# Optimization experiments

Hardware: AMD Instinct MI355X
Metric: run time of the kernel (lower is better)

Reference implementation:

```python
import jax, jax.numpy as jnp
import numpy as np

EPS = 1e-5


def _gcn_conv(h, W, b, src, dst, norm, N):
    # h: (B, N, F_in) -> linear transform then normalized neighbor aggregation
    h = h @ W                                  # (B, N, H)
    msg = h[:, src, :] * norm[None, :, None]   # gather + edge norm, (B, E, H)
    agg = jax.vmap(lambda m: jax.ops.segment_sum(m, dst, num_segments=N))(msg)
    return agg + b


def _batchnorm(h, gamma, beta):
    # BatchNorm1d over flattened (B*N, H), training-mode batch statistics
    B, N, H = h.shape
    f = h.reshape(-1, H)
    mean = f.mean(axis=0)
    var = f.var(axis=0)
    f = (f - mean) * jax.lax.rsqrt(var + EPS) * gamma + beta
    return f.reshape(B, N, H)


def setup_inputs() -> dict:
    key = jax.random.key(0)
    ks = jax.random.split(key, 6)
    B, N, E, IN, H, OUT = 2, 20000, 640000, 128, 128, 10
    x = jax.random.normal(ks[0], (B, N, IN), dtype=jnp.float32)
    edge_index = jax.random.randint(ks[1], (2, E), 0, N, dtype=jnp.int64)
    W1 = jax.random.normal(ks[2], (IN, H), dtype=jnp.float32) / np.sqrt(IN)
    W2 = jax.random.normal(ks[3], (H, H), dtype=jnp.float32) / np.sqrt(H)
    Wc = jax.random.normal(ks[4], (H, OUT), dtype=jnp.float32) / np.sqrt(H)
    return {
        "x": x,
        "W1": W1, "b1": jnp.zeros((H,), jnp.float32),
        "W2": W2, "b2": jnp.zeros((H,), jnp.float32),
        "g1": jnp.ones((H,), jnp.float32), "bt1": jnp.zeros((H,), jnp.float32),
        "g2": jnp.ones((H,), jnp.float32), "bt2": jnp.zeros((H,), jnp.float32),
        "Wc": Wc, "bc": jnp.zeros((OUT,), jnp.float32),
        "edge_index": edge_index,
    }


def reference(x, W1, b1, W2, b2, g1, bt1, g2, bt2, Wc, bc, edge_index):
    N = x.shape[1]
    loops = jnp.arange(N, dtype=edge_index.dtype)
    src = jnp.concatenate([edge_index[0], loops])  # add self-loops (GCNConv default)
    dst = jnp.concatenate([edge_index[1], loops])
    deg = jax.ops.segment_sum(jnp.ones(src.shape[0], x.dtype), dst, num_segments=N)
    dinv = jnp.where(deg > 0, jax.lax.rsqrt(deg), 0.0)
    norm = dinv[src] * dinv[dst]                   # symmetric GCN normalization

    h = jax.nn.relu(_gcn_conv(x, W1, b1, src, dst, norm, N))
    h = _batchnorm(h, g1, bt1)
    # dropout is identity in eval mode
    h = jax.nn.relu(_gcn_conv(h, W2, b2, src, dst, norm, N))
    h = _batchnorm(h, g2, bt2)
    return h @ Wc + bc                              # (B, N, out_dim)
```

## Files before the change

### kernel.cpp

```cpp
#include <hip/hip_runtime.h>
#include <hip/hip_bf16.h>


constexpr int Nn   = 20000;
constexpr int Ee   = 640000;
constexpr int OUTd = 10;
constexpr int Mm   = 2 * Nn;
constexpr int ELLW = 96;
constexpr int NSLOT = 64;
constexpr int SCB  = (Ee + 255) / 256;
constexpr int GMB  = Mm / 64;
#define EPSV 1e-5f
constexpr float INV_M = 1.0f / (float)Mm;

using frag16 = __attribute__((ext_vector_type(8))) short;
using f32x4  = __attribute__((ext_vector_type(4))) float;

__device__ inline short bf(float f) {
    union { __hip_bfloat16 h; short s; } u;
    u.h = __float2bfloat16(f);
    return u.s;
}
__device__ inline float lo16(unsigned u) { union { unsigned v; float f; } x; x.v = u << 16;        return x.f; }
__device__ inline float hi16(unsigned u) { union { unsigned v; float f; } x; x.v = u & 0xffff0000u; return x.f; }
__device__ inline unsigned pack2(float f0, float f1) {
    return (unsigned)(unsigned short)bf(f0) | ((unsigned)(unsigned short)bf(f1) << 16);
}

__global__ __launch_bounds__(256) void fg1_k(const int* __restrict__ src, const int* __restrict__ dst,
                                             int* __restrict__ cnt, int* __restrict__ ell,
                                             const float* __restrict__ A,
                                             const float* __restrict__ W,
                                             unsigned short* __restrict__ Hout) {
    __shared__ short Wl[128 * 136];
    int t = threadIdx.x;

    if (blockIdx.x < SCB) {
        int e = blockIdx.x * 256 + t;
        if (e < Ee) {
            int d = dst[e];
            int pos = atomicAdd(&cnt[d], 1);
            if (pos < ELLW) ell[(size_t)d * ELLW + pos] = src[e];
        }
        return;
    }

    int bid = blockIdx.x - SCB;

    for (int it = 0; it < 8; ++it) {
        int lin = it * 256 + t;
        int kp  = lin & 63;
        int n4  = (lin >> 6) * 4;
        float4 w0 = *(const float4*)(W + (size_t)(2 * kp) * 128 + n4);
        float4 w1 = *(const float4*)(W + (size_t)(2 * kp + 1) * 128 + n4);
        *(unsigned*)&Wl[(n4 + 0) * 136 + 2 * kp] = pack2(w0.x, w1.x);
        *(unsigned*)&Wl[(n4 + 1) * 136 + 2 * kp] = pack2(w0.y, w1.y);
        *(unsigned*)&Wl[(n4 + 2) * 136 + 2 * kp] = pack2(w0.z, w1.z);
        *(unsigned*)&Wl[(n4 + 3) * 136 + 2 * kp] = pack2(w0.w, w1.w);
    }
    __syncthreads();

    int wv = t >> 6, l = t & 63;
    int row_q = l >> 4, lane16 = l & 15;
    int row0 = bid * 64 + wv * 16;

    frag16 a[4];
    const float* Arow = A + (size_t)(row0 + lane16) * 128;
    #pragma unroll
    for (int q = 0; q < 4; ++q) {
        int k0 = q * 32 + row_q * 8;
        float4 v0 = *(const float4*)(Arow + k0);
        float4 v1 = *(const float4*)(Arow + k0 + 4);
        frag16 fa = { bf(v0.x), bf(v0.y), bf(v0.z), bf(v0.w),
                      bf(v1.x), bf(v1.y), bf(v1.z), bf(v1.w) };
        a[q] = fa;
    }

    f32x4 acc[8];
    #pragma unroll
    for (int c = 0; c < 8; ++c) acc[c] = (f32x4){0.f, 0.f, 0.f, 0.f};

    #pragma unroll
    for (int c = 0; c < 8; ++c) {
        int n = c * 16 + lane16;
        #pragma unroll
        for (int q = 0; q < 4; ++q) {
            int k0 = q * 32 + row_q * 8;
            frag16 b = *(const frag16*)&Wl[n * 136 + k0];
            acc[c] = __builtin_amdgcn_mfma_f32_16x16x32_bf16(a[q], b, acc[c], 0, 0, 0);
        }
    }

    #pragma unroll
    for (int r = 0; r < 4; ++r) {
        int rg = row0 + row_q * 4 + r;
        int b  = rg >= Nn;
        int n  = rg - b * Nn;
        unsigned short* dstp = Hout + (size_t)n * 256 + b * 128;
        #pragma unroll
        for (int c = 0; c < 8; ++c)
            dstp[c * 16 + lane16] = (unsigned short)bf(acc[c][r]);
    }
}

__global__ __launch_bounds__(256) void gemm2_k(const unsigned short* __restrict__ Abf,
                                               const float* __restrict__ W,
                                               const float* __restrict__ g,
                                               const float* __restrict__ bt,
                                               const float* __restrict__ S,
                                               unsigned short* __restrict__ Hout) {
    __shared__ short Wl[128 * 136];
    __shared__ float al[128], cl[128], dpart[2][128];
    int t = threadIdx.x;

    if (t < 128) {
        float s = 0.f, ss = 0.f;
        #pragma unroll 8
        for (int k = 0; k < NSLOT; ++k) {
            s  += S[k * 256 + t];
            ss += S[k * 256 + 128 + t];
        }
        float m   = s * INV_M;
        float var = ss * INV_M - m * m;
        float a   = g[t] * rsqrtf(var + EPSV);
        float c   = bt[t] - m * a;
        al[t] = a; cl[t] = c;
    }
    __syncthreads();

    for (int it = 0; it < 8; ++it) {
        int lin = it * 256 + t;
        int kp  = lin & 63;
        int n4  = (lin >> 6) * 4;
        float a0 = al[2 * kp], a1 = al[2 * kp + 1];
        float4 w0 = *(const float4*)(W + (size_t)(2 * kp) * 128 + n4);
        float4 w1 = *(const float4*)(W + (size_t)(2 * kp + 1) * 128 + n4);
        w0.x *= a0; w0.y *= a0; w0.z *= a0; w0.w *= a0;
        w1.x *= a1; w1.y *= a1; w1.z *= a1; w1.w *= a1;
        *(unsigned*)&Wl[(n4 + 0) * 136 + 2 * kp] = pack2(w0.x, w1.x);
        *(unsigned*)&Wl[(n4 + 1) * 136 + 2 * kp] = pack2(w0.y, w1.y);
        *(unsigned*)&Wl[(n4 + 2) * 136 + 2 * kp] = pack2(w0.z, w1.z);
        *(unsigned*)&Wl[(n4 + 3) * 136 + 2 * kp] = pack2(w0.w, w1.w);
    }

    {
        int col = t & 127, hh = t >> 7;
        const float* Wc0 = W + (size_t)(hh * 64) * 128 + col;
        float dp = 0.f;
        #pragma unroll 8
        for (int k = 0; k < 64; ++k) dp += cl[hh * 64 + k] * Wc0[(size_t)k * 128];
        dpart[hh][col] = dp;
    }
    __syncthreads();

    int wv = t >> 6, l = t & 63;
    int row_q = l >> 4, lane16 = l & 15;
    int row0 = blockIdx.x * 64 + wv * 16;

    int rgA = row0 + lane16;
    int bA  = rgA >= Nn;
    int nA  = rgA - bA * Nn;
    const unsigned short* Arow = Abf + (size_t)nA * 256 + bA * 128;
    frag16 a[4];
    #pragma unroll
    for (int q = 0; q < 4; ++q) {
        int k0 = q * 32 + row_q * 8;
        a[q] = *(const frag16*)(Arow + k0);
    }

    f32x4 acc[8];
    #pragma unroll
    for (int c = 0; c < 8; ++c) {
        int n = c * 16 + lane16;
        float d = dpart[0][n] + dpart[1][n];
        acc[c] = (f32x4){d, d, d, d};
    }

    #pragma unroll
    for (int c = 0; c < 8; ++c) {
        int n = c * 16 + lane16;
        #pragma unroll
        for (int q = 0; q < 4; ++q) {
            int k0 = q * 32 + row_q * 8;
            frag16 b = *(const frag16*)&Wl[n * 136 + k0];
            acc[c] = __builtin_amdgcn_mfma_f32_16x16x32_bf16(a[q], b, acc[c], 0, 0, 0);
        }
    }

    #pragma unroll
    for (int r = 0; r < 4; ++r) {
        int rg = row0 + row_q * 4 + r;
        int b  = rg >= Nn;
        int n  = rg - b * Nn;
        unsigned short* dst = Hout + (size_t)n * 256 + b * 128;
        #pragma unroll
        for (int c = 0; c < 8; ++c)
            dst[c * 16 + lane16] = (unsigned short)bf(acc[c][r]);
    }
}

__device__ inline void accw(const uint4& v, float w,
                            float& a0, float& a1, float& a2, float& a3,
                            float& a4, float& a5, float& a6, float& a7) {
    a0 = fmaf(w, lo16(v.x), a0); a1 = fmaf(w, hi16(v.x), a1);
    a2 = fmaf(w, lo16(v.y), a2); a3 = fmaf(w, hi16(v.y), a3);
    a4 = fmaf(w, lo16(v.z), a4); a5 = fmaf(w, hi16(v.z), a5);
    a6 = fmaf(w, lo16(v.w), a6); a7 = fmaf(w, hi16(v.w), a7);
}
__device__ inline float wdeg(int c) { return rsqrtf((float)c + 1.0f); }

__global__ __launch_bounds__(256) void agg_k(const unsigned short* __restrict__ h,
                                             const int* __restrict__ ell,
                                             const int* __restrict__ cnt,
                                             const float* __restrict__ bias,
                                             unsigned short* __restrict__ act,
                                             float* __restrict__ S) {
    int t  = threadIdx.x;
    int wv = t >> 6;
    int l  = t & 63;
    int n  = __builtin_amdgcn_readfirstlane(blockIdx.x * 4 + wv);
    int half = l >> 5;
    int g    = l & 31;

    const uint4* h4 = (const uint4*)h;

    float a0 = 0.f, a1 = 0.f, a2 = 0.f, a3 = 0.f, a4 = 0.f, a5 = 0.f, a6 = 0.f, a7 = 0.f;

    int degc = cnt[n];
    float dn = wdeg(degc);
    int deg = degc > ELLW ? ELLW : degc;
    const int* row = ell + (size_t)n * ELLW;

    uint4 u = h4[(size_t)n * 32 + g];

    int j = 0;
    for (; j + 15 < deg; j += 16) {
        int i0 = row[j +  0 + half], i1 = row[j +  2 + half];
        int i2 = row[j +  4 + half], i3 = row[j +  6 + half];
        int i4 = row[j +  8 + half], i5 = row[j + 10 + half];
        int i6 = row[j + 12 + half], i7 = row[j + 14 + half];
        int c0 = cnt[i0], c1 = cnt[i1], c2 = cnt[i2], c3 = cnt[i3];
        int c4 = cnt[i4], c5 = cnt[i5], c6 = cnt[i6], c7 = cnt[i7];
        uint4 v0 = h4[(size_t)i0 * 32 + g];
        uint4 v1 = h4[(size_t)i1 * 32 + g];
        uint4 v2 = h4[(size_t)i2 * 32 + g];
        uint4 v3 = h4[(size_t)i3 * 32 + g];
        uint4 v4 = h4[(size_t)i4 * 32 + g];
        uint4 v5 = h4[(size_t)i5 * 32 + g];
        uint4 v6 = h4[(size_t)i6 * 32 + g];
        uint4 v7 = h4[(size_t)i7 * 32 + g];
        accw(v0, wdeg(c0), a0, a1, a2, a3, a4, a5, a6, a7);
        accw(v1, wdeg(c1), a0, a1, a2, a3, a4, a5, a6, a7);
        accw(v2, wdeg(c2), a0, a1, a2, a3, a4, a5, a6, a7);
        accw(v3, wdeg(c3), a0, a1, a2, a3, a4, a5, a6, a7);
        accw(v4, wdeg(c4), a0, a1, a2, a3, a4, a5, a6, a7);
        accw(v5, wdeg(c5), a0, a1, a2, a3, a4, a5, a6, a7);
        accw(v6, wdeg(c6), a0, a1, a2, a3, a4, a5, a6, a7);
        accw(v7, wdeg(c7), a0, a1, a2, a3, a4, a5, a6, a7);
    }
    for (; j + 3 < deg; j += 4) {
        int i0 = row[j + half];
        int i1 = row[j + 2 + half];
        int c0 = cnt[i0], c1 = cnt[i1];
        uint4 v0 = h4[(size_t)i0 * 32 + g];
        uint4 v1 = h4[(size_t)i1 * 32 + g];
        accw(v0, wdeg(c0), a0, a1, a2, a3, a4, a5, a6, a7);
        accw(v1, wdeg(c1), a0, a1, a2, a3, a4, a5, a6, a7);
    }
    for (; j + 1 < deg; j += 2) {
        int i0 = row[j + half];
        int c0 = cnt[i0];
        uint4 v0 = h4[(size_t)i0 * 32 + g];
        accw(v0, wdeg(c0), a0, a1, a2, a3, a4, a5, a6, a7);
    }
    if (j < deg) {
        if (half == 0) {
            int i0 = row[j];
            int c0 = cnt[i0];
            uint4 v0 = h4[(size_t)i0 * 32 + g];
            accw(v0, wdeg(c0), a0, a1, a2, a3, a4, a5, a6, a7);
        }
    }

    a0 += __shfl_xor(a0, 32); a1 += __shfl_xor(a1, 32);
    a2 += __shfl_xor(a2, 32); a3 += __shfl_xor(a3, 32);
    a4 += __shfl_xor(a4, 32); a5 += __shfl_xor(a5, 32);
    a6 += __shfl_xor(a6, 32); a7 += __shfl_xor(a7, 32);

    int cb   = (g & 15) * 8;
    float4 b0 = *(const float4*)(bias + cb);
    float4 b1 = *(const float4*)(bias + cb + 4);
    float i0v = fmaf(dn, lo16(u.x), a0), i1v = fmaf(dn, hi16(u.x), a1);
    float i2v = fmaf(dn, lo16(u.y), a2), i3v = fmaf(dn, hi16(u.y), a3);
    float i4v = fmaf(dn, lo16(u.z), a4), i5v = fmaf(dn, hi16(u.z), a5);
    float i6v = fmaf(dn, lo16(u.w), a6), i7v = fmaf(dn, hi16(u.w), a7);
    float o0 = fmaxf(fmaf(dn, i0v, b0.x), 0.f);
    float o1 = fmaxf(fmaf(dn, i1v, b0.y), 0.f);
    float o2 = fmaxf(fmaf(dn, i2v, b0.z), 0.f);
    float o3 = fmaxf(fmaf(dn, i3v, b0.w), 0.f);
    float o4 = fmaxf(fmaf(dn, i4v, b1.x), 0.f);
    float o5 = fmaxf(fmaf(dn, i5v, b1.y), 0.f);
    float o6 = fmaxf(fmaf(dn, i6v, b1.z), 0.f);
    float o7 = fmaxf(fmaf(dn, i7v, b1.w), 0.f);

    if (l < 32) {
        uint4 st;
        st.x = pack2(o0, o1); st.y = pack2(o2, o3);
        st.z = pack2(o4, o5); st.w = pack2(o6, o7);
        *(uint4*)(act + (size_t)n * 256 + (size_t)g * 8) = st;
    }

    float q0 = o0 * o0, q1 = o1 * o1, q2 = o2 * o2, q3 = o3 * o3;
    float q4 = o4 * o4, q5 = o5 * o5, q6 = o6 * o6, q7 = o7 * o7;
    float s0 = o0 + __shfl_xor(o0, 16), s1 = o1 + __shfl_xor(o1, 16);
    float s2 = o2 + __shfl_xor(o2, 16), s3 = o3 + __shfl_xor(o3, 16);
    float s4 = o4 + __shfl_xor(o4, 16), s5 = o5 + __shfl_xor(o5, 16);
    float s6 = o6 + __shfl_xor(o6, 16), s7 = o7 + __shfl_xor(o7, 16);
    float t0 = q0 + __shfl_xor(q0, 16), t1 = q1 + __shfl_xor(q1, 16);
    float t2 = q2 + __shfl_xor(q2, 16), t3 = q3 + __shfl_xor(q3, 16);
    float t4 = q4 + __shfl_xor(q4, 16), t5 = q5 + __shfl_xor(q5, 16);
    float t6 = q6 + __shfl_xor(q6, 16), t7 = q7 + __shfl_xor(q7, 16);

    __shared__ float sh[4][16][17];
    if (l < 16) {
        float* p = sh[wv][l];
        p[0] = s0; p[1] = s1; p[2] = s2; p[3] = s3;
        p[4] = s4; p[5] = s5; p[6] = s6; p[7] = s7;
        p[8]  = t0; p[9]  = t1; p[10] = t2; p[11] = t3;
        p[12] = t4; p[13] = t5; p[14] = t6; p[15] = t7;
    }
    __syncthreads();
    int col  = t & 127, stat = t >> 7;
    int gi   = col >> 3, slot = (col & 7) + stat * 8;
    float v = sh[0][gi][slot] + sh[1][gi][slot] + sh[2][gi][slot] + sh[3][gi][slot];
    atomicAdd(&S[(blockIdx.x & (NSLOT - 1)) * 256 + stat * 128 + col], v);
}

__global__ __launch_bounds__(256) void gemmout_k(const unsigned short* __restrict__ act,
                                                 const float* __restrict__ Wc,
                                                 const float* __restrict__ bc,
                                                 const float* __restrict__ g,
                                                 const float* __restrict__ bt,
                                                 const float* __restrict__ S,
                                                 float* __restrict__ out) {
    __shared__ float Wl[128 * OUTd];
    __shared__ float bl[OUTd];
    __shared__ float al[128], cl[128];
    int t = threadIdx.x;
    for (int i = t; i < 128 * OUTd; i += 256) Wl[i] = Wc[i];
    if (t < OUTd) bl[t] = bc[t];
    if (t < 128) {
        float s = 0.f, ss = 0.f;
        #pragma unroll 8
        for (int k = 0; k < NSLOT; ++k) {
            s  += S[k * 256 + t];
            ss += S[k * 256 + 128 + t];
        }
        float m   = s * INV_M;
        float var = ss * INV_M - m * m;
        float a   = g[t] * rsqrtf(var + EPSV);
        al[t] = a;
        cl[t] = bt[t] - m * a;
    }
    __syncthreads();

    int r = blockIdx.x * 256 + t;
    if (r >= Mm) return;
    int b = r >= Nn;
    int n = r - b * Nn;

    float acc[OUTd];
    #pragma unroll
    for (int jj = 0; jj < OUTd; jj++) acc[jj] = 0.f;

    const uint4* a4 = (const uint4*)(act + (size_t)n * 256 + b * 128);
    #pragma unroll 4
    for (int k4 = 0; k4 < 16; k4++) {
        uint4 u = a4[k4];
        int k = k4 * 8;
        float e0 = lo16(u.x) * al[k+0] + cl[k+0];
        float e1 = hi16(u.x) * al[k+1] + cl[k+1];
        float e2 = lo16(u.y) * al[k+2] + cl[k+2];
        float e3 = hi16(u.y) * al[k+3] + cl[k+3];
        float e4 = lo16(u.z) * al[k+4] + cl[k+4];
        float e5 = hi16(u.z) * al[k+5] + cl[k+5];
        float e6 = lo16(u.w) * al[k+6] + cl[k+6];
        float e7 = hi16(u.w) * al[k+7] + cl[k+7];
        #pragma unroll
        for (int jj = 0; jj < OUTd; jj++) {
            acc[jj] += e0 * Wl[(k+0) * OUTd + jj];
            acc[jj] += e1 * Wl[(k+1) * OUTd + jj];
            acc[jj] += e2 * Wl[(k+2) * OUTd + jj];
            acc[jj] += e3 * Wl[(k+3) * OUTd + jj];
            acc[jj] += e4 * Wl[(k+4) * OUTd + jj];
            acc[jj] += e5 * Wl[(k+5) * OUTd + jj];
            acc[jj] += e6 * Wl[(k+6) * OUTd + jj];
            acc[jj] += e7 * Wl[(k+7) * OUTd + jj];
        }
    }
    #pragma unroll
    for (int jj = 0; jj < OUTd; jj++) out[(size_t)r * OUTd + jj] = acc[jj] + bl[jj];
}

extern "C" void kernel_launch(void* const* d_in, const int* in_sizes, int n_in,
                              void* d_out, int out_size, void* d_ws, size_t ws_size,
                              hipStream_t stream) {
    (void)in_sizes; (void)n_in; (void)out_size; (void)ws_size;

    const float* x   = (const float*)d_in[0];
    const float* W1  = (const float*)d_in[1];
    const float* b1  = (const float*)d_in[2];
    const float* W2  = (const float*)d_in[3];
    const float* b2  = (const float*)d_in[4];
    const float* g1  = (const float*)d_in[5];
    const float* bt1 = (const float*)d_in[6];
    const float* g2  = (const float*)d_in[7];
    const float* bt2 = (const float*)d_in[8];
    const float* Wc  = (const float*)d_in[9];
    const float* bc  = (const float*)d_in[10];
    const int*   ei  = (const int*)d_in[11];
    const int* srcp = ei;
    const int* dstp = ei + Ee;

    char* ws = (char*)d_ws;
    size_t off = 0;
    auto alloc = [&](size_t bytes) -> void* {
        void* p = ws + off;
        off += (bytes + 511) & ~(size_t)511;
        return p;
    };
    unsigned short* h   = (unsigned short*)alloc((size_t)Mm * 128 * 2);
    unsigned short* act = (unsigned short*)alloc((size_t)Mm * 128 * 2);
    int*   cnt  = (int*)alloc(Nn * 4 + 2 * NSLOT * 256 * 4);
    float* S1   = (float*)(cnt + Nn);
    float* S2   = S1 + NSLOT * 256;
    int*   ell  = (int*)alloc((size_t)Nn * ELLW * 4);

    float* out = (float*)d_out;

    hipMemsetAsync(cnt, 0, Nn * 4 + 2 * NSLOT * 256 * 4, stream);
    fg1_k<<<SCB + GMB, 256, 0, stream>>>(srcp, dstp, cnt, ell, x, W1, h);

    agg_k<<<Nn / 4, 256, 0, stream>>>(h, ell, cnt, b1, act, S1);

    gemm2_k<<<Mm / 64, 256, 0, stream>>>(act, W2, g1, bt1, S1, h);
    agg_k<<<Nn / 4, 256, 0, stream>>>(h, ell, cnt, b2, act, S2);

    gemmout_k<<<(Mm + 255) / 256, 256, 0, stream>>>(act, Wc, bc, g2, bt2, S2, out);
}
```

Baseline: 245.4 us.

## Pre-scale layer-2 features by source degree and partition ELL build by destination range

The second GEMM now multiplies each output row by its node's inverse-sqrt degree, so the layer-2 aggregation sums neighbour rows without reading per-neighbour counts or computing rsqrt. This removes one dependent gather of cnt per edge in that kernel. The ELL construction blocks now each scan 2048 edges and keep only destinations in one of eight node ranges, which gives better atomic locality per block but reads the dst array eight times. GEMM blocks are now placed ahead of the scatter blocks in the fused launch.

```diff
diff --git a/kernel.cpp b/kernel.cpp
--- a/kernel.cpp
+++ b/kernel.cpp
@@ -8,7 +8,10 @@
 constexpr int Mm   = 2 * Nn;
 constexpr int ELLW = 96;
 constexpr int NSLOT = 64;
-constexpr int SCB  = (Ee + 255) / 256;
+constexpr int NP   = 8;
+constexpr int PSZ  = Nn / NP;
+constexpr int NSEG = (Ee + 2047) / 2048;
+constexpr int SCB  = NSEG * NP;
 constexpr int GMB  = Mm / 64;
 #define EPSV 1e-5f
 constexpr float INV_M = 1.0f / (float)Mm;
@@ -26,6 +29,7 @@
 __device__ inline unsigned pack2(float f0, float f1) {
     return (unsigned)(unsigned short)bf(f0) | ((unsigned)(unsigned short)bf(f1) << 16);
 }
+__device__ inline float wdeg(int c) { return rsqrtf((float)c + 1.0f); }
 
 __global__ __launch_bounds__(256) void fg1_k(const int* __restrict__ src, const int* __restrict__ dst,
                                              int* __restrict__ cnt, int* __restrict__ ell,
@@ -35,17 +39,27 @@
     __shared__ short Wl[128 * 136];
     int t = threadIdx.x;
 
-    if (blockIdx.x < SCB) {
-        int e = blockIdx.x * 256 + t;
-        if (e < Ee) {
-            int d = dst[e];
-            int pos = atomicAdd(&cnt[d], 1);
-            if (pos < ELLW) ell[(size_t)d * ELLW + pos] = src[e];
+    if (blockIdx.x >= GMB) {
+        int s   = blockIdx.x - GMB;
+        int p   = blockIdx.x & 7;
+        int seg = s >> 3;
+        int lo  = p * PSZ, hi = lo + PSZ;
+        int base = seg * 2048 + t;
+        #pragma unroll
+        for (int it = 0; it < 8; ++it) {
+            int e = base + it * 256;
+            if (e < Ee) {
+                int d = dst[e];
+                if (d >= lo && d < hi) {
+                    int pos = atomicAdd(&cnt[d], 1);
+                    if (pos < ELLW) ell[(size_t)d * ELLW + pos] = src[e];
+                }
+            }
         }
         return;
     }
 
-    int bid = blockIdx.x - SCB;
+    int bid = blockIdx.x;
 
     for (int it = 0; it < 8; ++it) {
         int lin = it * 256 + t;
@@ -108,6 +122,7 @@
                                                const float* __restrict__ g,
                                                const float* __restrict__ bt,
                                                const float* __restrict__ S,
+                                               const int* __restrict__ cnt,
                                                unsigned short* __restrict__ Hout) {
     __shared__ short Wl[128 * 136];
     __shared__ float al[128], cl[128], dpart[2][128];
@@ -192,10 +207,11 @@
         int rg = row0 + row_q * 4 + r;
         int b  = rg >= Nn;
         int n  = rg - b * Nn;
+        float dv = wdeg(cnt[n]);
         unsigned short* dst = Hout + (size_t)n * 256 + b * 128;
         #pragma unroll
         for (int c = 0; c < 8; ++c)
-            dst[c * 16 + lane16] = (unsigned short)bf(acc[c][r]);
+            dst[c * 16 + lane16] = (unsigned short)bf(acc[c][r] * dv);
     }
 }
 
@@ -207,14 +223,51 @@
     a4 = fmaf(w, lo16(v.z), a4); a5 = fmaf(w, hi16(v.z), a5);
     a6 = fmaf(w, lo16(v.w), a6); a7 = fmaf(w, hi16(v.w), a7);
 }
-__device__ inline float wdeg(int c) { return rsqrtf((float)c + 1.0f); }
-
-__global__ __launch_bounds__(256) void agg_k(const unsigned short* __restrict__ h,
-                                             const int* __restrict__ ell,
-                                             const int* __restrict__ cnt,
-                                             const float* __restrict__ bias,
-                                             unsigned short* __restrict__ act,
-                                             float* __restrict__ S) {
+__device__ inline void acc8(const uint4& v,
+                            float& a0, float& a1, float& a2, float& a3,
+                            float& a4, float& a5, float& a6, float& a7) {
+    a0 += lo16(v.x); a1 += hi16(v.x);
+    a2 += lo16(v.y); a3 += hi16(v.y);
+    a4 += lo16(v.z); a5 += hi16(v.z);
+    a6 += lo16(v.w); a7 += hi16(v.w);
+}
+
+__device__ inline void stats_epilogue(int t, int wv, int l, int g, unsigned bslot,
+                                      float o0, float o1, float o2, float o3,
+                                      float o4, float o5, float o6, float o7,
+                                      float* __restrict__ S) {
+    float q0 = o0 * o0, q1 = o1 * o1, q2 = o2 * o2, q3 = o3 * o3;
+    float q4 = o4 * o4, q5 = o5 * o5, q6 = o6 * o6, q7 = o7 * o7;
+    float s0 = o0 + __shfl_xor(o0, 16), s1 = o1 + __shfl_xor(o1, 16);
+    float s2 = o2 + __shfl_xor(o2, 16), s3 = o3 + __shfl_xor(o3, 16);
+    float s4 = o4 + __shfl_xor(o4, 16), s5 = o5 + __shfl_xor(o5, 16);
+    float s6 = o6 + __shfl_xor(o6, 16), s7 = o7 + __shfl_xor(o7, 16);
+    float t0 = q0 + __shfl_xor(q0, 16), t1 = q1 + __shfl_xor(q1, 16);
+    float t2 = q2 + __shfl_xor(q2, 16), t3 = q3 + __shfl_xor(q3, 16);
+    float t4 = q4 + __shfl_xor(q4, 16), t5 = q5 + __shfl_xor(q5, 16);
+    float t6 = q6 + __shfl_xor(q6, 16), t7 = q7 + __shfl_xor(q7, 16);
+
+    __shared__ float sh[4][16][17];
+    if (l < 16) {
+        float* p = sh[wv][l];
+        p[0] = s0; p[1] = s1; p[2] = s2; p[3] = s3;
+        p[4] = s4; p[5] = s5; p[6] = s6; p[7] = s7;
+        p[8]  = t0; p[9]  = t1; p[10] = t2; p[11] = t3;
+        p[12] = t4; p[13] = t5; p[14] = t6; p[15] = t7;
+    }
+    __syncthreads();
+    int col  = t & 127, stat = t >> 7;
+    int gi   = col >> 3, slot = (col & 7) + stat * 8;
+    float v = sh[0][gi][slot] + sh[1][gi][slot] + sh[2][gi][slot] + sh[3][gi][slot];
+    atomicAdd(&S[bslot * 256 + stat * 128 + col], v);
+}
+
+__global__ __launch_bounds__(256) void agg1_k(const unsigned short* __restrict__ h,
+                                              const int* __restrict__ ell,
+                                              const int* __restrict__ cnt,
+                                              const float* __restrict__ bias,
+                                              unsigned short* __restrict__ act,
+                                              float* __restrict__ S) {
     int t  = threadIdx.x;
     int wv = t >> 6;
     int l  = t & 63;
@@ -273,13 +326,11 @@
         uint4 v0 = h4[(size_t)i0 * 32 + g];
         accw(v0, wdeg(c0), a0, a1, a2, a3, a4, a5, a6, a7);
     }
-    if (j < deg) {
-        if (half == 0) {
-            int i0 = row[j];
-            int c0 = cnt[i0];
-            uint4 v0 = h4[(size_t)i0 * 32 + g];
-            accw(v0, wdeg(c0), a0, a1, a2, a3, a4, a5, a6, a7);
-        }
+    if (j < deg && half == 0) {
+        int i0 = row[j];
+        int c0 = cnt[i0];
+        uint4 v0 = h4[(size_t)i0 * 32 + g];
+        accw(v0, wdeg(c0), a0, a1, a2, a3, a4, a5, a6, a7);
     }
 
     a0 += __shfl_xor(a0, 32); a1 += __shfl_xor(a1, 32);
@@ -310,30 +361,102 @@
         *(uint4*)(act + (size_t)n * 256 + (size_t)g * 8) = st;
     }
 
-    float q0 = o0 * o0, q1 = o1 * o1, q2 = o2 * o2, q3 = o3 * o3;
-    float q4 = o4 * o4, q5 = o5 * o5, q6 = o6 * o6, q7 = o7 * o7;
-    float s0 = o0 + __shfl_xor(o0, 16), s1 = o1 + __shfl_xor(o1, 16);
-    float s2 = o2 + __shfl_xor(o2, 16), s3 = o3 + __shfl_xor(o3, 16);
-    float s4 = o4 + __shfl_xor(o4, 16), s5 = o5 + __shfl_xor(o5, 16);
-    float s6 = o6 + __shfl_xor(o6, 16), s7 = o7 + __shfl_xor(o7, 16);
-    float t0 = q0 + __shfl_xor(q0, 16), t1 = q1 + __shfl_xor(q1, 16);
-    float t2 = q2 + __shfl_xor(q2, 16), t3 = q3 + __shfl_xor(q3, 16);
-    float t4 = q4 + __shfl_xor(q4, 16), t5 = q5 + __shfl_xor(q5, 16);
-    float t6 = q6 + __shfl_xor(q6, 16), t7 = q7 + __shfl_xor(q7, 16);
-
-    __shared__ float sh[4][16][17];
-    if (l < 16) {
-        float* p = sh[wv][l];
-        p[0] = s0; p[1] = s1; p[2] = s2; p[3] = s3;
-        p[4] = s4; p[5] = s5; p[6] = s6; p[7] = s7;
-        p[8]  = t0; p[9]  = t1; p[10] = t2; p[11] = t3;
-        p[12] = t4; p[13] = t5; p[14] = t6; p[15] = t7;
-    }
-    __syncthreads();
-    int col  = t & 127, stat = t >> 7;
-    int gi   = col >> 3, slot = (col & 7) + stat * 8;
-    float v = sh[0][gi][slot] + sh[1][gi][slot] + sh[2][gi][slot] + sh[3][gi][slot];
-    atomicAdd(&S[(blockIdx.x & (NSLOT - 1)) * 256 + stat * 128 + col], v);
+    stats_epilogue(t, wv, l, g, blockIdx.x & (NSLOT - 1),
+                   o0, o1, o2, o3, o4, o5, o6, o7, S);
+}
+
+__global__ __launch_bounds__(256) void agg2_k(const unsigned short* __restrict__ h,
+                                              const int* __restrict__ ell,
+                                              const int* __restrict__ cnt,
+                                              const float* __restrict__ bias,
+                                              unsigned short* __restrict__ act,
+                                              float* __restrict__ S) {
+    int t  = threadIdx.x;
+    int wv = t >> 6;
+    int l  = t & 63;
+    int n  = __builtin_amdgcn_readfirstlane(blockIdx.x * 4 + wv);
+    int half = l >> 5;
+    int g    = l & 31;
+
+    const uint4* h4 = (const uint4*)h;
+
+    float a0 = 0.f, a1 = 0.f, a2 = 0.f, a3 = 0.f, a4 = 0.f, a5 = 0.f, a6 = 0.f, a7 = 0.f;
+
+    int degc = cnt[n];
+    float dn = wdeg(degc);
+    int deg = degc > ELLW ? ELLW : degc;
+    const int* row = ell + (size_t)n * ELLW;
+
+    uint4 u = h4[(size_t)n * 32 + g];
+
+    int j = 0;
+    for (; j + 15 < deg; j += 16) {
+        int i0 = row[j +  0 + half], i1 = row[j +  2 + half];
+        int i2 = row[j +  4 + half], i3 = row[j +  6 + half];
+        int i4 = row[j +  8 + half], i5 = row[j + 10 + half];
+        int i6 = row[j + 12 + half], i7 = row[j + 14 + half];
+        uint4 v0 = h4[(size_t)i0 * 32 + g];
+        uint4 v1 = h4[(size_t)i1 * 32 + g];
+        uint4 v2 = h4[(size_t)i2 * 32 + g];
+        uint4 v3 = h4[(size_t)i3 * 32 + g];
+        uint4 v4 = h4[(size_t)i4 * 32 + g];
+        uint4 v5 = h4[(size_t)i5 * 32 + g];
+        uint4 v6 = h4[(size_t)i6 * 32 + g];
+        uint4 v7 = h4[(size_t)i7 * 32 + g];
+        acc8(v0, a0, a1, a2, a3, a4, a5, a6, a7);
+        acc8(v1, a0, a1, a2, a3, a4, a5, a6, a7);
+        acc8(v2, a0, a1, a2, a3, a4, a5, a6, a7);
+        acc8(v3, a0, a1, a2, a3, a4, a5, a6, a7);
+        acc8(v4, a0, a1, a2, a3, a4, a5, a6, a7);
+        acc8(v5, a0, a1, a2, a3, a4, a5, a6, a7);
+        acc8(v6, a0, a1, a2, a3, a4, a5, a6, a7);
+        acc8(v7, a0, a1, a2, a3, a4, a5, a6, a7);
+    }
+    for (; j + 3 < deg; j += 4) {
+        int i0 = row[j + half];
+        int i1 = row[j + 2 + half];
+        uint4 v0 = h4[(size_t)i0 * 32 + g];
+        uint4 v1 = h4[(size_t)i1 * 32 + g];
+        acc8(v0, a0, a1, a2, a3, a4, a5, a6, a7);
+        acc8(v1, a0, a1, a2, a3, a4, a5, a6, a7);
+    }
+    for (; j + 1 < deg; j += 2) {
+        int i0 = row[j + half];
+        uint4 v0 = h4[(size_t)i0 * 32 + g];
+        acc8(v0, a0, a1, a2, a3, a4, a5, a6, a7);
+    }
+    if (j < deg && half == 0) {
+        int i0 = row[j];
+        uint4 v0 = h4[(size_t)i0 * 32 + g];
+        acc8(v0, a0, a1, a2, a3, a4, a5, a6, a7);
+    }
+
+    a0 += __shfl_xor(a0, 32); a1 += __shfl_xor(a1, 32);
+    a2 += __shfl_xor(a2, 32); a3 += __shfl_xor(a3, 32);
+    a4 += __shfl_xor(a4, 32); a5 += __shfl_xor(a5, 32);
+    a6 += __shfl_xor(a6, 32); a7 += __shfl_xor(a7, 32);
+
+    int cb   = (g & 15) * 8;
+    float4 b0 = *(const float4*)(bias + cb);
+    float4 b1 = *(const float4*)(bias + cb + 4);
+    float o0 = fmaxf(fmaf(dn, a0 + lo16(u.x), b0.x), 0.f);
+    float o1 = fmaxf(fmaf(dn, a1 + hi16(u.x), b0.y), 0.f);
+    float o2 = fmaxf(fmaf(dn, a2 + lo16(u.y), b0.z), 0.f);
+    float o3 = fmaxf(fmaf(dn, a3 + hi16(u.y), b0.w), 0.f);
+    float o4 = fmaxf(fmaf(dn, a4 + lo16(u.z), b1.x), 0.f);
+    float o5 = fmaxf(fmaf(dn, a5 + hi16(u.z), b1.y), 0.f);
+    float o6 = fmaxf(fmaf(dn, a6 + lo16(u.w), b1.z), 0.f);
+    float o7 = fmaxf(fmaf(dn, a7 + hi16(u.w), b1.w), 0.f);
+
+    if (l < 32) {
+        uint4 st;
+        st.x = pack2(o0, o1); st.y = pack2(o2, o3);
+        st.z = pack2(o4, o5); st.w = pack2(o6, o7);
+        *(uint4*)(act + (size_t)n * 256 + (size_t)g * 8) = st;
+    }
+
+    stats_epilogue(t, wv, l, g, blockIdx.x & (NSLOT - 1),
+                   o0, o1, o2, o3, o4, o5, o6, o7, S);
 }
 
 __global__ __launch_bounds__(256) void gemmout_k(const unsigned short* __restrict__ act,
@@ -439,12 +562,12 @@
     float* out = (float*)d_out;
 
     hipMemsetAsync(cnt, 0, Nn * 4 + 2 * NSLOT * 256 * 4, stream);
-    fg1_k<<<SCB + GMB, 256, 0, stream>>>(srcp, dstp, cnt, ell, x, W1, h);
-
-    agg_k<<<Nn / 4, 256, 0, stream>>>(h, ell, cnt, b1, act, S1);
-
-    gemm2_k<<<Mm / 64, 256, 0, stream>>>(act, W2, g1, bt1, S1, h);
-    agg_k<<<Nn / 4, 256, 0, stream>>>(h, ell, cnt, b2, act, S2);
+    fg1_k<<<GMB + SCB, 256, 0, stream>>>(srcp, dstp, cnt, ell, x, W1, h);
+
+    agg1_k<<<Nn / 4, 256, 0, stream>>>(h, ell, cnt, b1, act, S1);
+
+    gemm2_k<<<Mm / 64, 256, 0, stream>>>(act, W2, g1, bt1, S1, cnt, h);
+    agg2_k<<<Nn / 4, 256, 0, stream>>>(h, ell, cnt, b2, act, S2);
 
     gemmout_k<<<(Mm + 255) / 256, 256, 0, stream>>>(act, Wc, bc, g2, bt2, S2, out);
 }
```

Measured after the change: 241.1 us (median of 2 runs). About the same (-1.8%).

## Bucket edges by destination partition, fold source norm into GEMM2, feature-partitioned aggregation

Applied to the files above, without the earlier changes.

Edge scatter into the ELL table now runs in two passes. Edges are first bucketed by destination range into 8 partitions using block-local atomics, and a separate kernel then does the per-node atomics, so atomic traffic is localized. The second layer's source-degree weight is folded into the GEMM2 epilogue, which lets the second aggregation skip per-neighbor degree loads. Aggregation is restructured so each block handles one 32-column feature slice for 8 nodes, with 16 edges gathered in parallel per wave, to improve cache locality of gathers. This adds an extra kernel launch, a pairs buffer capped at PCAP per partition, and more total index reads, since each node's row is reread for each of the 8 feature slices.

```diff
diff --git a/kernel.cpp b/kernel.cpp
--- a/kernel.cpp
+++ b/kernel.cpp
@@ -8,8 +8,12 @@
 constexpr int Mm   = 2 * Nn;
 constexpr int ELLW = 96;
 constexpr int NSLOT = 64;
-constexpr int SCB  = (Ee + 255) / 256;
+constexpr int NP   = 8;
+constexpr int PSZ  = Nn / NP;
+constexpr int PCAP = 98304;
 constexpr int GMB  = Mm / 64;
+constexpr int BKB  = (Ee + 1023) / 1024;
+constexpr int PBB  = 96;
 #define EPSV 1e-5f
 constexpr float INV_M = 1.0f / (float)Mm;
 
@@ -26,26 +30,46 @@
 __device__ inline unsigned pack2(float f0, float f1) {
     return (unsigned)(unsigned short)bf(f0) | ((unsigned)(unsigned short)bf(f1) << 16);
 }
+__device__ inline float wdeg(int c) { return rsqrtf((float)c + 1.0f); }
 
 __global__ __launch_bounds__(256) void fg1_k(const int* __restrict__ src, const int* __restrict__ dst,
-                                             int* __restrict__ cnt, int* __restrict__ ell,
+                                             int* __restrict__ cursor, uint2* __restrict__ pairs,
                                              const float* __restrict__ A,
                                              const float* __restrict__ W,
                                              unsigned short* __restrict__ Hout) {
     __shared__ short Wl[128 * 136];
+    __shared__ int pcnt[NP];
+    __shared__ int pbase[NP];
     int t = threadIdx.x;
 
-    if (blockIdx.x < SCB) {
-        int e = blockIdx.x * 256 + t;
-        if (e < Ee) {
+    if (blockIdx.x >= GMB) {
+        int s  = blockIdx.x - GMB;
+        int e0 = s * 1024;
+        if (t < NP) pcnt[t] = 0;
+        __syncthreads();
+        int es[4], ed[4], pp[4], pos[4];
+        #pragma unroll
+        for (int it = 0; it < 4; ++it) {
+            int e = e0 + it * 256 + t;
             int d = dst[e];
-            int pos = atomicAdd(&cnt[d], 1);
-            if (pos < ELLW) ell[(size_t)d * ELLW + pos] = src[e];
+            es[it] = src[e];
+            ed[it] = d;
+            pp[it] = (int)((unsigned)d / (unsigned)PSZ);
+            pos[it] = atomicAdd(&pcnt[pp[it]], 1);
+        }
+        __syncthreads();
+        if (t < NP) pbase[t] = atomicAdd(&cursor[t], pcnt[t]);
+        __syncthreads();
+        #pragma unroll
+        for (int it = 0; it < 4; ++it) {
+            int idx = pbase[pp[it]] + pos[it];
+            if (idx < PCAP)
+                pairs[(size_t)pp[it] * PCAP + idx] = make_uint2((unsigned)es[it], (unsigned)ed[it]);
         }
         return;
     }
 
-    int bid = blockIdx.x - SCB;
+    int bid = blockIdx.x;
 
     for (int it = 0; it < 8; ++it) {
         int lin = it * 256 + t;
@@ -103,11 +127,27 @@
     }
 }
 
+__global__ __launch_bounds__(256) void scat2_k(const uint2* __restrict__ pairs,
+                                               const int* __restrict__ cursor,
+                                               int* __restrict__ cnt, int* __restrict__ ell) {
+    int p     = blockIdx.x & (NP - 1);
+    int chunk = blockIdx.x >> 3;
+    int m = cursor[p]; if (m > PCAP) m = PCAP;
+    const uint2* bk = pairs + (size_t)p * PCAP;
+    for (int i = chunk * 256 + threadIdx.x; i < m; i += PBB * 256) {
+        uint2 pr = bk[i];
+        int d = (int)pr.y;
+        int pos = atomicAdd(&cnt[d], 1);
+        if (pos < ELLW) ell[(size_t)d * ELLW + pos] = (int)pr.x;
+    }
+}
+
 __global__ __launch_bounds__(256) void gemm2_k(const unsigned short* __restrict__ Abf,
                                                const float* __restrict__ W,
                                                const float* __restrict__ g,
                                                const float* __restrict__ bt,
                                                const float* __restrict__ S,
+                                               const int* __restrict__ cnt,
                                                unsigned short* __restrict__ Hout) {
     __shared__ short Wl[128 * 136];
     __shared__ float al[128], cl[128], dpart[2][128];
@@ -192,148 +232,163 @@
         int rg = row0 + row_q * 4 + r;
         int b  = rg >= Nn;
         int n  = rg - b * Nn;
+        float dv = wdeg(cnt[n]);
         unsigned short* dst = Hout + (size_t)n * 256 + b * 128;
         #pragma unroll
         for (int c = 0; c < 8; ++c)
-            dst[c * 16 + lane16] = (unsigned short)bf(acc[c][r]);
-    }
-}
-
-__device__ inline void accw(const uint4& v, float w,
-                            float& a0, float& a1, float& a2, float& a3,
-                            float& a4, float& a5, float& a6, float& a7) {
-    a0 = fmaf(w, lo16(v.x), a0); a1 = fmaf(w, hi16(v.x), a1);
-    a2 = fmaf(w, lo16(v.y), a2); a3 = fmaf(w, hi16(v.y), a3);
-    a4 = fmaf(w, lo16(v.z), a4); a5 = fmaf(w, hi16(v.z), a5);
-    a6 = fmaf(w, lo16(v.w), a6); a7 = fmaf(w, hi16(v.w), a7);
-}
-__device__ inline float wdeg(int c) { return rsqrtf((float)c + 1.0f); }
-
-__global__ __launch_bounds__(256) void agg_k(const unsigned short* __restrict__ h,
-                                             const int* __restrict__ ell,
-                                             const int* __restrict__ cnt,
-                                             const float* __restrict__ bias,
-                                             unsigned short* __restrict__ act,
-                                             float* __restrict__ S) {
-    int t  = threadIdx.x;
-    int wv = t >> 6;
-    int l  = t & 63;
-    int n  = __builtin_amdgcn_readfirstlane(blockIdx.x * 4 + wv);
-    int half = l >> 5;
-    int g    = l & 31;
-
+            dst[c * 16 + lane16] = (unsigned short)bf(acc[c][r] * dv);
+    }
+}
+
+template<int WEIGHTED>
+__global__ __launch_bounds__(256) void aggs_k(const unsigned short* __restrict__ h,
+                                              const int* __restrict__ ell,
+                                              const int* __restrict__ cnt,
+                                              const float* __restrict__ bias,
+                                              unsigned short* __restrict__ act,
+                                              float* __restrict__ S) {
+    int t    = threadIdx.x;
+    int wv   = t >> 6;
+    int l    = t & 63;
+    int p    = blockIdx.x & 7;
+    int ng   = blockIdx.x >> 3;
+    int esub = l >> 2;
+    int c4   = l & 3;
+    int uo   = p * 4 + c4;
     const uint4* h4 = (const uint4*)h;
-
-    float a0 = 0.f, a1 = 0.f, a2 = 0.f, a3 = 0.f, a4 = 0.f, a5 = 0.f, a6 = 0.f, a7 = 0.f;
-
-    int degc = cnt[n];
-    float dn = wdeg(degc);
-    int deg = degc > ELLW ? ELLW : degc;
-    const int* row = ell + (size_t)n * ELLW;
-
-    uint4 u = h4[(size_t)n * 32 + g];
-
-    int j = 0;
-    for (; j + 15 < deg; j += 16) {
-        int i0 = row[j +  0 + half], i1 = row[j +  2 + half];
-        int i2 = row[j +  4 + half], i3 = row[j +  6 + half];
-        int i4 = row[j +  8 + half], i5 = row[j + 10 + half];
-        int i6 = row[j + 12 + half], i7 = row[j + 14 + half];
-        int c0 = cnt[i0], c1 = cnt[i1], c2 = cnt[i2], c3 = cnt[i3];
-        int c4 = cnt[i4], c5 = cnt[i5], c6 = cnt[i6], c7 = cnt[i7];
-        uint4 v0 = h4[(size_t)i0 * 32 + g];
-        uint4 v1 = h4[(size_t)i1 * 32 + g];
-        uint4 v2 = h4[(size_t)i2 * 32 + g];
-        uint4 v3 = h4[(size_t)i3 * 32 + g];
-        uint4 v4 = h4[(size_t)i4 * 32 + g];
-        uint4 v5 = h4[(size_t)i5 * 32 + g];
-        uint4 v6 = h4[(size_t)i6 * 32 + g];
-        uint4 v7 = h4[(size_t)i7 * 32 + g];
-        accw(v0, wdeg(c0), a0, a1, a2, a3, a4, a5, a6, a7);
-        accw(v1, wdeg(c1), a0, a1, a2, a3, a4, a5, a6, a7);
-        accw(v2, wdeg(c2), a0, a1, a2, a3, a4, a5, a6, a7);
-        accw(v3, wdeg(c3), a0, a1, a2, a3, a4, a5, a6, a7);
-        accw(v4, wdeg(c4), a0, a1, a2, a3, a4, a5, a6, a7);
-        accw(v5, wdeg(c5), a0, a1, a2, a3, a4, a5, a6, a7);
-        accw(v6, wdeg(c6), a0, a1, a2, a3, a4, a5, a6, a7);
-        accw(v7, wdeg(c7), a0, a1, a2, a3, a4, a5, a6, a7);
-    }
-    for (; j + 3 < deg; j += 4) {
-        int i0 = row[j + half];
-        int i1 = row[j + 2 + half];
-        int c0 = cnt[i0], c1 = cnt[i1];
-        uint4 v0 = h4[(size_t)i0 * 32 + g];
-        uint4 v1 = h4[(size_t)i1 * 32 + g];
-        accw(v0, wdeg(c0), a0, a1, a2, a3, a4, a5, a6, a7);
-        accw(v1, wdeg(c1), a0, a1, a2, a3, a4, a5, a6, a7);
-    }
-    for (; j + 1 < deg; j += 2) {
-        int i0 = row[j + half];
-        int c0 = cnt[i0];
-        uint4 v0 = h4[(size_t)i0 * 32 + g];
-        accw(v0, wdeg(c0), a0, a1, a2, a3, a4, a5, a6, a7);
-    }
-    if (j < deg) {
-        if (half == 0) {
-            int i0 = row[j];
-            int c0 = cnt[i0];
-            uint4 v0 = h4[(size_t)i0 * 32 + g];
-            accw(v0, wdeg(c0), a0, a1, a2, a3, a4, a5, a6, a7);
-        }
-    }
-
-    a0 += __shfl_xor(a0, 32); a1 += __shfl_xor(a1, 32);
-    a2 += __shfl_xor(a2, 32); a3 += __shfl_xor(a3, 32);
-    a4 += __shfl_xor(a4, 32); a5 += __shfl_xor(a5, 32);
-    a6 += __shfl_xor(a6, 32); a7 += __shfl_xor(a7, 32);
-
-    int cb   = (g & 15) * 8;
-    float4 b0 = *(const float4*)(bias + cb);
-    float4 b1 = *(const float4*)(bias + cb + 4);
-    float i0v = fmaf(dn, lo16(u.x), a0), i1v = fmaf(dn, hi16(u.x), a1);
-    float i2v = fmaf(dn, lo16(u.y), a2), i3v = fmaf(dn, hi16(u.y), a3);
-    float i4v = fmaf(dn, lo16(u.z), a4), i5v = fmaf(dn, hi16(u.z), a5);
-    float i6v = fmaf(dn, lo16(u.w), a6), i7v = fmaf(dn, hi16(u.w), a7);
-    float o0 = fmaxf(fmaf(dn, i0v, b0.x), 0.f);
-    float o1 = fmaxf(fmaf(dn, i1v, b0.y), 0.f);
-    float o2 = fmaxf(fmaf(dn, i2v, b0.z), 0.f);
-    float o3 = fmaxf(fmaf(dn, i3v, b0.w), 0.f);
-    float o4 = fmaxf(fmaf(dn, i4v, b1.x), 0.f);
-    float o5 = fmaxf(fmaf(dn, i5v, b1.y), 0.f);
-    float o6 = fmaxf(fmaf(dn, i6v, b1.z), 0.f);
-    float o7 = fmaxf(fmaf(dn, i7v, b1.w), 0.f);
-
-    if (l < 32) {
-        uint4 st;
-        st.x = pack2(o0, o1); st.y = pack2(o2, o3);
-        st.z = pack2(o4, o5); st.w = pack2(o6, o7);
-        *(uint4*)(act + (size_t)n * 256 + (size_t)g * 8) = st;
-    }
-
-    float q0 = o0 * o0, q1 = o1 * o1, q2 = o2 * o2, q3 = o3 * o3;
-    float q4 = o4 * o4, q5 = o5 * o5, q6 = o6 * o6, q7 = o7 * o7;
-    float s0 = o0 + __shfl_xor(o0, 16), s1 = o1 + __shfl_xor(o1, 16);
-    float s2 = o2 + __shfl_xor(o2, 16), s3 = o3 + __shfl_xor(o3, 16);
-    float s4 = o4 + __shfl_xor(o4, 16), s5 = o5 + __shfl_xor(o5, 16);
-    float s6 = o6 + __shfl_xor(o6, 16), s7 = o7 + __shfl_xor(o7, 16);
-    float t0 = q0 + __shfl_xor(q0, 16), t1 = q1 + __shfl_xor(q1, 16);
-    float t2 = q2 + __shfl_xor(q2, 16), t3 = q3 + __shfl_xor(q3, 16);
-    float t4 = q4 + __shfl_xor(q4, 16), t5 = q5 + __shfl_xor(q5, 16);
-    float t6 = q6 + __shfl_xor(q6, 16), t7 = q7 + __shfl_xor(q7, 16);
-
-    __shared__ float sh[4][16][17];
-    if (l < 16) {
-        float* p = sh[wv][l];
-        p[0] = s0; p[1] = s1; p[2] = s2; p[3] = s3;
-        p[4] = s4; p[5] = s5; p[6] = s6; p[7] = s7;
-        p[8]  = t0; p[9]  = t1; p[10] = t2; p[11] = t3;
-        p[12] = t4; p[13] = t5; p[14] = t6; p[15] = t7;
+    int cb   = (p & 3) * 32 + c4 * 8;
+
+    float oS[8] = {0.f,0.f,0.f,0.f,0.f,0.f,0.f,0.f};
+    float qS[8] = {0.f,0.f,0.f,0.f,0.f,0.f,0.f,0.f};
+
+    for (int s = 0; s < 2; ++s) {
+        int n = __builtin_amdgcn_readfirstlane(ng * 8 + wv * 2 + s);
+        int degc = cnt[n];
+        float dn = wdeg(degc);
+        int deg = degc > ELLW ? ELLW : degc;
+        const int* row = ell + (size_t)n * ELLW;
+
+        uint4 u = h4[(size_t)n * 32 + uo];
+
+        float a0 = 0.f, a1 = 0.f, a2 = 0.f, a3 = 0.f;
+        float a4 = 0.f, a5 = 0.f, a6 = 0.f, a7 = 0.f;
+
+        int j = 0;
+        for (; j + 32 <= deg; j += 32) {
+            int i0 = row[j + esub];
+            int i1 = row[j + 16 + esub];
+            float w0 = 1.f, w1 = 1.f;
+            if (WEIGHTED) { w0 = wdeg(cnt[i0]); w1 = wdeg(cnt[i1]); }
+            uint4 v0 = h4[(size_t)i0 * 32 + uo];
+            uint4 v1 = h4[(size_t)i1 * 32 + uo];
+            if (WEIGHTED) {
+                a0 = fmaf(w0, lo16(v0.x), a0); a1 = fmaf(w0, hi16(v0.x), a1);
+                a2 = fmaf(w0, lo16(v0.y), a2); a3 = fmaf(w0, hi16(v0.y), a3);
+                a4 = fmaf(w0, lo16(v0.z), a4); a5 = fmaf(w0, hi16(v0.z), a5);
+                a6 = fmaf(w0, lo16(v0.w), a6); a7 = fmaf(w0, hi16(v0.w), a7);
+                a0 = fmaf(w1, lo16(v1.x), a0); a1 = fmaf(w1, hi16(v1.x), a1);
+                a2 = fmaf(w1, lo16(v1.y), a2); a3 = fmaf(w1, hi16(v1.y), a3);
+                a4 = fmaf(w1, lo16(v1.z), a4); a5 = fmaf(w1, hi16(v1.z), a5);
+                a6 = fmaf(w1, lo16(v1.w), a6); a7 = fmaf(w1, hi16(v1.w), a7);
+            } else {
+                a0 += lo16(v0.x); a1 += hi16(v0.x); a2 += lo16(v0.y); a3 += hi16(v0.y);
+                a4 += lo16(v0.z); a5 += hi16(v0.z); a6 += lo16(v0.w); a7 += hi16(v0.w);
+                a0 += lo16(v1.x); a1 += hi16(v1.x); a2 += lo16(v1.y); a3 += hi16(v1.y);
+                a4 += lo16(v1.z); a5 += hi16(v1.z); a6 += lo16(v1.w); a7 += hi16(v1.w);
+            }
+        }
+        for (; j + 16 <= deg; j += 16) {
+            int i0 = row[j + esub];
+            float w0 = 1.f;
+            if (WEIGHTED) w0 = wdeg(cnt[i0]);
+            uint4 v0 = h4[(size_t)i0 * 32 + uo];
+            if (WEIGHTED) {
+                a0 = fmaf(w0, lo16(v0.x), a0); a1 = fmaf(w0, hi16(v0.x), a1);
+                a2 = fmaf(w0, lo16(v0.y), a2); a3 = fmaf(w0, hi16(v0.y), a3);
+                a4 = fmaf(w0, lo16(v0.z), a4); a5 = fmaf(w0, hi16(v0.z), a5);
+                a6 = fmaf(w0, lo16(v0.w), a6); a7 = fmaf(w0, hi16(v0.w), a7);
+            } else {
+                a0 += lo16(v0.x); a1 += hi16(v0.x); a2 += lo16(v0.y); a3 += hi16(v0.y);
+                a4 += lo16(v0.z); a5 += hi16(v0.z); a6 += lo16(v0.w); a7 += hi16(v0.w);
+            }
+        }
+        if (j < deg) {
+            int e = j + esub;
+            if (e < deg) {
+                int i0 = row[e];
+                float w0 = 1.f;
+                if (WEIGHTED) w0 = wdeg(cnt[i0]);
+                uint4 v0 = h4[(size_t)i0 * 32 + uo];
+                if (WEIGHTED) {
+                    a0 = fmaf(w0, lo16(v0.x), a0); a1 = fmaf(w0, hi16(v0.x), a1);
+                    a2 = fmaf(w0, lo16(v0.y), a2); a3 = fmaf(w0, hi16(v0.y), a3);
+                    a4 = fmaf(w0, lo16(v0.z), a4); a5 = fmaf(w0, hi16(v0.z), a5);
+                    a6 = fmaf(w0, lo16(v0.w), a6); a7 = fmaf(w0, hi16(v0.w), a7);
+                } else {
+                    a0 += lo16(v0.x); a1 += hi16(v0.x); a2 += lo16(v0.y); a3 += hi16(v0.y);
+                    a4 += lo16(v0.z); a5 += hi16(v0.z); a6 += lo16(v0.w); a7 += hi16(v0.w);
+                }
+            }
+        }
+
+        #pragma unroll
+        for (int m = 4; m <= 32; m <<= 1) {
+            a0 += __shfl_xor(a0, m); a1 += __shfl_xor(a1, m);
+            a2 += __shfl_xor(a2, m); a3 += __shfl_xor(a3, m);
+            a4 += __shfl_xor(a4, m); a5 += __shfl_xor(a5, m);
+            a6 += __shfl_xor(a6, m); a7 += __shfl_xor(a7, m);
+        }
+
+        if (l < 4) {
+            float4 b0 = *(const float4*)(bias + cb);
+            float4 b1 = *(const float4*)(bias + cb + 4);
+            float o0, o1, o2, o3, o4, o5, o6, o7;
+            if (WEIGHTED) {
+                o0 = fmaxf(fmaf(dn, fmaf(dn, lo16(u.x), a0), b0.x), 0.f);
+                o1 = fmaxf(fmaf(dn, fmaf(dn, hi16(u.x), a1), b0.y), 0.f);
+                o2 = fmaxf(fmaf(dn, fmaf(dn, lo16(u.y), a2), b0.z), 0.f);
+                o3 = fmaxf(fmaf(dn, fmaf(dn, hi16(u.y), a3), b0.w), 0.f);
+                o4 = fmaxf(fmaf(dn, fmaf(dn, lo16(u.z), a4), b1.x), 0.f);
+                o5 = fmaxf(fmaf(dn, fmaf(dn, hi16(u.z), a5), b1.y), 0.f);
+                o6 = fmaxf(fmaf(dn, fmaf(dn, lo16(u.w), a6), b1.z), 0.f);
+                o7 = fmaxf(fmaf(dn, fmaf(dn, hi16(u.w), a7), b1.w), 0.f);
+            } else {
+                o0 = fmaxf(fmaf(dn, a0 + lo16(u.x), b0.x), 0.f);
+                o1 = fmaxf(fmaf(dn, a1 + hi16(u.x), b0.y), 0.f);
+                o2 = fmaxf(fmaf(dn, a2 + lo16(u.y), b0.z), 0.f);
+                o3 = fmaxf(fmaf(dn, a3 + hi16(u.y), b0.w), 0.f);
+                o4 = fmaxf(fmaf(dn, a4 + lo16(u.z), b1.x), 0.f);
+                o5 = fmaxf(fmaf(dn, a5 + hi16(u.z), b1.y), 0.f);
+                o6 = fmaxf(fmaf(dn, a6 + lo16(u.w), b1.z), 0.f);
+                o7 = fmaxf(fmaf(dn, a7 + hi16(u.w), b1.w), 0.f);
+            }
+            uint4 st;
+            st.x = pack2(o0, o1); st.y = pack2(o2, o3);
+            st.z = pack2(o4, o5); st.w = pack2(o6, o7);
+            *(uint4*)(act + (size_t)n * 256 + (size_t)p * 32 + (size_t)c4 * 8) = st;
+
+            oS[0] += o0; oS[1] += o1; oS[2] += o2; oS[3] += o3;
+            oS[4] += o4; oS[5] += o5; oS[6] += o6; oS[7] += o7;
+            qS[0] += o0*o0; qS[1] += o1*o1; qS[2] += o2*o2; qS[3] += o3*o3;
+            qS[4] += o4*o4; qS[5] += o5*o5; qS[6] += o6*o6; qS[7] += o7*o7;
+        }
+    }
+
+    __shared__ float sh[4][4][16];
+    if (l < 4) {
+        float* ptr = sh[wv][l];
+        #pragma unroll
+        for (int k = 0; k < 8; ++k) { ptr[k] = oS[k]; ptr[8 + k] = qS[k]; }
     }
     __syncthreads();
-    int col  = t & 127, stat = t >> 7;
-    int gi   = col >> 3, slot = (col & 7) + stat * 8;
-    float v = sh[0][gi][slot] + sh[1][gi][slot] + sh[2][gi][slot] + sh[3][gi][slot];
-    atomicAdd(&S[(blockIdx.x & (NSLOT - 1)) * 256 + stat * 128 + col], v);
+    if (t < 64) {
+        int c = t >> 4;
+        int k = t & 15;
+        float v = sh[0][c][k] + sh[1][c][k] + sh[2][c][k] + sh[3][c][k];
+        int col  = (p & 3) * 32 + c * 8 + (k & 7);
+        int stat = k >> 3;
+        atomicAdd(&S[((blockIdx.x >> 3) & (NSLOT - 1)) * 256 + stat * 128 + col], v);
+    }
 }
 
 __global__ __launch_bounds__(256) void gemmout_k(const unsigned short* __restrict__ act,
@@ -431,20 +486,24 @@
     };
     unsigned short* h   = (unsigned short*)alloc((size_t)Mm * 128 * 2);
     unsigned short* act = (unsigned short*)alloc((size_t)Mm * 128 * 2);
-    int*   cnt  = (int*)alloc(Nn * 4 + 2 * NSLOT * 256 * 4);
+    int*   cnt  = (int*)alloc(Nn * 4 + 2 * NSLOT * 256 * 4 + NP * 4);
     float* S1   = (float*)(cnt + Nn);
     float* S2   = S1 + NSLOT * 256;
+    int*   cursor = (int*)(S2 + NSLOT * 256);
     int*   ell  = (int*)alloc((size_t)Nn * ELLW * 4);
+    uint2* pairs = (uint2*)alloc((size_t)NP * PCAP * 8);
 
     float* out = (float*)d_out;
 
-    hipMemsetAsync(cnt, 0, Nn * 4 + 2 * NSLOT * 256 * 4, stream);
-    fg1_k<<<SCB + GMB, 256, 0, stream>>>(srcp, dstp, cnt, ell, x, W1, h);
-
-    agg_k<<<Nn / 4, 256, 0, stream>>>(h, ell, cnt, b1, act, S1);
-
-    gemm2_k<<<Mm / 64, 256, 0, stream>>>(act, W2, g1, bt1, S1, h);
-    agg_k<<<Nn / 4, 256, 0, stream>>>(h, ell, cnt, b2, act, S2);
+    hipMemsetAsync(cnt, 0, Nn * 4 + 2 * NSLOT * 256 * 4 + NP * 4, stream);
+    fg1_k<<<GMB + BKB, 256, 0, stream>>>(srcp, dstp, cursor, pairs, x, W1, h);
+
+    scat2_k<<<NP * PBB, 256, 0, stream>>>(pairs, cursor, cnt, ell);
+
+    aggs_k<1><<<(Nn / 8) * 8, 256, 0, stream>>>(h, ell, cnt, b1, act, S1);
+
+    gemm2_k<<<Mm / 64, 256, 0, stream>>>(act, W2, g1, bt1, S1, cnt, h);
+    aggs_k<0><<<(Nn / 8) * 8, 256, 0, stream>>>(h, ell, cnt, b2, act, S2);
 
     gemmout_k<<<(Mm + 255) / 256, 256, 0, stream>>>(act, Wc, bc, g2, bt2, S2, out);
 }
```

Result: slower. 296.5 us (+20.8%).
